# Optimization experiments

Hardware: AMD Instinct MI355X
Metric: run time of the kernel (lower is better)

Reference implementation:

```python
import jax, jax.numpy as jnp
import numpy as np

HIDDEN = 1024
HEADS = 16
HEAD_DIM = HIDDEN // HEADS


def setup_inputs() -> dict:
    key = jax.random.key(0)
    kx, kw = jax.random.split(key)
    x = jax.random.normal(kx, (1, 4096, HIDDEN), dtype=jnp.float32)
    # torch Linear weight is [out, in]; we store as [in, out] for x @ W
    W_qkv = jax.random.normal(kw, (HIDDEN, 3 * HIDDEN), dtype=jnp.float32) * (HIDDEN ** -0.5)
    return {"x": x, "W_qkv": W_qkv}


def reference(x, W_qkv):
    B, T, _ = x.shape
    qkv = x @ W_qkv                                    # [B, T, 3*HIDDEN]
    qkv = qkv.reshape(B, T, 3, HEADS, HEAD_DIM)
    qkv = jnp.transpose(qkv, (2, 0, 3, 1, 4))          # [3, B, H, T, Dh]
    q, k, v = qkv[0], qkv[1], qkv[2]
    scale = HEAD_DIM ** -0.5
    attn = jnp.einsum("bhqd,bhkd->bhqk", q, k) * scale  # [B, H, T, T] materialized (naive)
    attn = jax.nn.softmax(attn, axis=-1)
    out = jnp.einsum("bhqk,bhkd->bhqd", attn, v)        # [B, H, T, Dh]
    out = jnp.transpose(out, (0, 2, 1, 3)).reshape(B, T, HIDDEN)
    return out
```

## Files before the change

kernel.cpp:

```cpp
#include <hip/hip_runtime.h>

#define SEQ 4096
#define HID 1024
#define NH  16
#define DH  64
#define N3  3072

typedef __attribute__((ext_vector_type(4))) float floatx4;
typedef __attribute__((ext_vector_type(8))) short shortx8;
typedef __attribute__((ext_vector_type(4))) short shortx4;

__device__ __forceinline__ short f2bf(float f) {
    return (short)((__builtin_bit_cast(unsigned, f) + 0x8000u) >> 16);
}
__device__ __forceinline__ unsigned pk2bf(float a, float b) {
    unsigned ua = __builtin_bit_cast(unsigned, a) + 0x8000u;
    unsigned ub = __builtin_bit_cast(unsigned, b) + 0x8000u;
    return (ua >> 16) | (ub & 0xFFFF0000u);
}
__device__ __forceinline__ shortx4 pk4bf(float a, float b, float c, float d) {
    union { unsigned u[2]; shortx4 s; } x;
    x.u[0] = pk2bf(a, b);
    x.u[1] = pk2bf(c, d);
    return x.s;
}

__device__ __forceinline__ unsigned cvtpk(float lo, float hi) {
    unsigned r;
    asm("v_cvt_pk_bf16_f32 %0, %1, %2" : "=v"(r) : "v"(lo), "v"(hi));
    return r;
}

#if __has_builtin(__builtin_amdgcn_exp2f)
#define fexp2 __builtin_amdgcn_exp2f
#else
#define fexp2 exp2f
#endif

#define mfma32 __builtin_amdgcn_mfma_f32_16x16x32_bf16

__device__ __forceinline__ void gll16(const short* g, short* l) {
    __builtin_amdgcn_global_load_lds(
        (const __attribute__((address_space(1))) unsigned*)g,
        (__attribute__((address_space(3))) unsigned*)l, 16, 0, 0);
}

__global__ __launch_bounds__(256) void prep(
    const float* __restrict__ x, const float* __restrict__ W,
    short* __restrict__ Xb, short* __restrict__ Wt)
{
    __shared__ short Ws[128 * 40];
    const int t = threadIdx.x;
    if (blockIdx.x < 4096) {
        size_t i = (size_t)blockIdx.x * 256 + t;
        float4 v = *(const float4*)&x[i * 4];
        *(shortx4*)&Xb[i * 4] = pk4bf(v.x, v.y, v.z, v.w);
        return;
    }
    const int bx = (int)blockIdx.x - 4096;
    const int n0 = (bx % 24) * 128;
    const int k0 = (bx / 24) * 32;
    #pragma unroll
    for (int i = 0; i < 4; i++) {
        int idx = t + i * 256;
        int k = idx >> 5, c4 = idx & 31;
        float4 v = *(const float4*)&W[(size_t)(k0 + k) * N3 + n0 + c4 * 4];
        Ws[(c4 * 4 + 0) * 40 + k] = f2bf(v.x);
        Ws[(c4 * 4 + 1) * 40 + k] = f2bf(v.y);
        Ws[(c4 * 4 + 2) * 40 + k] = f2bf(v.z);
        Ws[(c4 * 4 + 3) * 40 + k] = f2bf(v.w);
    }
    __syncthreads();
    #pragma unroll
    for (int i = 0; i < 2; i++) {
        int idx = t + i * 256;
        int n = idx >> 2, seg = idx & 3;
        shortx8 g = *(const shortx8*)&Ws[n * 40 + seg * 8];
        *(shortx8*)&Wt[(size_t)(n0 + n) * HID + k0 + seg * 8] = g;
    }
}

#define LDC 136
__global__ __launch_bounds__(256) void qkv_gemm(
    const short* __restrict__ Xb, const short* __restrict__ Wt,
    short* __restrict__ Qb, short* __restrict__ Kb, short* __restrict__ Vt)
{
    __shared__ short SM[18432];
    short* As = SM;
    short* Bs = SM + 128 * 64;
    const int tid  = threadIdx.x;
    const int m0   = blockIdx.x * 128;
    const int n0   = blockIdx.y * 128;
    const int lane = tid & 63;
    const int wid  = tid >> 6;
    const int wm   = (wid >> 1) * 64;
    const int wn   = (wid & 1) * 64;
    const int l15  = lane & 15;
    const int quad = lane >> 4;

    floatx4 acc[4][4];
    #pragma unroll
    for (int i = 0; i < 4; i++)
        #pragma unroll
        for (int j = 0; j < 4; j++)
            acc[i][j] = (floatx4){0.f, 0.f, 0.f, 0.f};

    const int arow = tid >> 3, ac = tid & 7;
    const int swk  = (ac ^ (arow & 7)) << 3;
    const short* ag = Xb + (size_t)(m0 + arow) * HID + swk;
    const short* bg = Wt + (size_t)(n0 + arow) * HID + swk;
    short* al = As + (size_t)(tid & 192) * 8;
    short* bl = Bs + (size_t)(tid & 192) * 8;
    const int r7 = l15 & 7;

    for (int k0 = 0; k0 < HID; k0 += 64) {
        #pragma unroll
        for (int i = 0; i < 4; i++)
            gll16(ag + (size_t)i * 32 * HID + k0, al + i * 2048);
        #pragma unroll
        for (int i = 0; i < 4; i++)
            gll16(bg + (size_t)i * 32 * HID + k0, bl + i * 2048);
        __syncthreads();
        #pragma unroll
        for (int kh = 0; kh < 2; kh++) {
            shortx8 af[4], bf[4];
            #pragma unroll
            for (int t = 0; t < 4; t++) {
                int R = wm + t * 16 + l15;
                af[t] = *(const shortx8*)&As[(R << 6) + ((((kh << 2) + quad) ^ r7) << 3)];
                int Rb = wn + t * 16 + l15;
                bf[t] = *(const shortx8*)&Bs[(Rb << 6) + ((((kh << 2) + quad) ^ r7) << 3)];
            }
            #pragma unroll
            for (int tm = 0; tm < 4; tm++)
                #pragma unroll
                for (int tn = 0; tn < 4; tn++)
                    acc[tm][tn] = mfma32(af[tm], bf[tn], acc[tm][tn], 0, 0, 0);
        }
        __syncthreads();
    }

    short* Cs = SM;
    const float sc = (n0 < 1024) ? 0.18033688011112042f : 1.0f;
    #pragma unroll
    for (int tm = 0; tm < 4; tm++)
        #pragma unroll
        for (int tn = 0; tn < 4; tn++)
            #pragma unroll
            for (int r = 0; r < 4; r++)
                Cs[(wm + tm * 16 + quad * 4 + r) * LDC + wn + tn * 16 + l15] =
                    f2bf(acc[tm][tn][r] * sc);
    __syncthreads();
    const int h0 = (n0 & 1023) >> 6;
    if (n0 < 2048) {
        short* base = (n0 < 1024) ? Qb : Kb;
        #pragma unroll
        for (int j = 0; j < 8; j++) {
            int idx = tid + j * 256;
            int row = idx >> 4, col = (idx & 15) * 8;
            shortx8 v = *(const shortx8*)&Cs[row * LDC + col];
            *(shortx8*)&base[((size_t)(h0 + (col >> 6)) * SEQ + m0 + row) * DH + (col & 63)] = v;
        }
    } else {
        #pragma unroll
        for (int j = 0; j < 8; j++) {
            int idx = tid + j * 256;
            int col = idx >> 4;
            int t8  = (idx & 15) * 8;
            shortx8 v;
            #pragma unroll
            for (int k = 0; k < 8; k++) v[k] = Cs[(t8 + k) * LDC + col];
            *(shortx8*)&Vt[((size_t)(h0 + (col >> 6)) * DH + (col & 63)) * SEQ + m0 + t8] = v;
        }
    }
}

__global__ __launch_bounds__(256, 3) void flash_attn(
    const short* __restrict__ Qb, const short* __restrict__ Kb,
    const short* __restrict__ Vt, float* __restrict__ out,
    float* __restrict__ Opart, float* __restrict__ Lpart,
    int chn, int final)
{
    __shared__ short Ks[2][4096];
    __shared__ short Vs[2][4096];
    const int tid  = threadIdx.x;
    const int wid  = tid >> 6;
    const int lane = tid & 63;
    const int l15  = lane & 15;
    const int quad = lane >> 4;

    const int nblk = (int)(gridDim.x * gridDim.y * gridDim.z);
    const int lin  = (int)blockIdx.x + ((int)blockIdx.y << 4) + ((int)blockIdx.z << 8);
    const int work = (lin & 7) * (nblk >> 3) + (lin >> 3);
    const int h    = (work >> 4) & 15;
    const int ch   = work >> 8;
    const int q0   = (work & 15) * 256 + wid * 64;
    const int nit    = (chn == 1) ? 64 : (ch == 0 ? 22 : 21);
    const int tstart = (chn == 1) ? 0  : (ch == 0 ? 0 : 1408 + (ch - 1) * 1344);
    const shortx8 ones8 = {(short)0x3F80, (short)0x3F80, (short)0x3F80, (short)0x3F80,
                           (short)0x3F80, (short)0x3F80, (short)0x3F80, (short)0x3F80};
    const floatx4 z4 = {0.f, 0.f, 0.f, 0.f};

    shortx8 qf[4][2];
    #pragma unroll
    for (int s = 0; s < 4; s++) {
        const short* qp = Qb + ((size_t)h * SEQ + q0 + s * 16 + l15) * DH;
        qf[s][0] = *(const shortx8*)(qp + quad * 8);
        qf[s][1] = *(const shortx8*)(qp + 32 + quad * 8);
    }

    floatx4 oacc[4][4];
    #pragma unroll
    for (int s = 0; s < 4; s++)
        #pragma unroll
        for (int dn = 0; dn < 4; dn++)
            oacc[s][dn] = z4;
    floatx4 lacc[4] = {z4, z4, z4, z4};

    const int rK   = tid >> 3, sK = tid & 7;
    const int key0 = 8 * ((rK >> 2) & 3) + 4 * ((rK >> 4) & 1) + (rK & 3);
    const int swo  = (sK ^ (rK & 7)) << 3;
    const short* kg = Kb + ((size_t)h * SEQ + tstart + key0) * DH + swo;
    const short* vg = Vt + ((size_t)h * DH + rK) * SEQ + tstart + swo;
    const int wslot = (tid & 192) * 8;

#define STAGE(b) do { \
        gll16(kg,            &Ks[b][wslot]); \
        gll16(kg + 32 * DH,  &Ks[b][wslot + 2048]); \
        gll16(vg,            &Vs[b][wslot]); \
        gll16(vg + 32 * SEQ, &Vs[b][wslot + 2048]); \
    } while (0)

    STAGE(0);
    kg += 64 * DH;  vg += 64;

    for (int it = 0; it < nit; it++) {
        __syncthreads();
        if (it + 1 < nit) {
            int b = (it + 1) & 1;
            STAGE(b);
            kg += 64 * DH;  vg += 64;
        }
        const short* ks = Ks[it & 1];
        const short* vs = Vs[it & 1];

        #pragma unroll
        for (int pair = 0; pair < 2; pair++) {
            int Ra = (pair * 2) * 16 + l15;
            int Rb = Ra + 16;
            int offa = (Ra << 6) + ((quad ^ (Ra & 7)) << 3);
            int offb = (Rb << 6) + ((quad ^ (Rb & 7)) << 3);
            shortx8 kf0a = *(const shortx8*)&ks[offa];
            shortx8 kf1a = *(const shortx8*)&ks[offa ^ 32];
            shortx8 kf0b = *(const shortx8*)&ks[offb];
            shortx8 kf1b = *(const shortx8*)&ks[offb ^ 32];
            floatx4 sta[4], stb[4];
            __builtin_amdgcn_s_setprio(1);
            #pragma unroll
            for (int s = 0; s < 4; s++) {
                floatx4 a = mfma32(kf0a, qf[s][0], z4, 0, 0, 0);
                a = mfma32(kf1a, qf[s][1], a, 0, 0, 0);
                sta[s] = a;
                floatx4 b = mfma32(kf0b, qf[s][0], z4, 0, 0, 0);
                b = mfma32(kf1b, qf[s][1], b, 0, 0, 0);
                stb[s] = b;
            }
            __builtin_amdgcn_s_setprio(0);
            union { unsigned u[4]; shortx8 s8; } pa[4];
            #pragma unroll
            for (int s = 0; s < 4; s++) {
                pa[s].u[0] = cvtpk(fexp2(sta[s][0]), fexp2(sta[s][1]));
                pa[s].u[1] = cvtpk(fexp2(sta[s][2]), fexp2(sta[s][3]));
                pa[s].u[2] = cvtpk(fexp2(stb[s][0]), fexp2(stb[s][1]));
                pa[s].u[3] = cvtpk(fexp2(stb[s][2]), fexp2(stb[s][3]));
            }
            __builtin_amdgcn_s_setprio(1);
            #pragma unroll
            for (int s = 0; s < 4; s++)
                lacc[s] = mfma32(pa[s].s8, ones8, lacc[s], 0, 0, 0);
            #pragma unroll
            for (int dn = 0; dn < 4; dn++) {
                int row = dn * 16 + l15;
                int off = ((row << 6) + ((quad ^ (row & 7)) << 3)) ^ (pair << 5);
                shortx8 vv = *(const shortx8*)&vs[off];
                #pragma unroll
                for (int s = 0; s < 4; s++)
                    oacc[s][dn] = mfma32(pa[s].s8, vv, oacc[s][dn], 0, 0, 0);
            }
            __builtin_amdgcn_s_setprio(0);
        }
    }
#undef STAGE

    if (final) {
        #pragma unroll
        for (int s = 0; s < 4; s++)
            #pragma unroll
            for (int r = 0; r < 4; r++) {
                float rl = 1.0f / lacc[s][r];
                int query = q0 + s * 16 + quad * 4 + r;
                float* d = out + (size_t)query * HID + h * DH + l15;
                #pragma unroll
                for (int dn = 0; dn < 4; dn++)
                    d[dn * 16] = oacc[s][dn][r] * rl;
            }
    } else {
        #pragma unroll
        for (int s = 0; s < 4; s++)
            #pragma unroll
            for (int r = 0; r < 4; r++) {
                int query = q0 + s * 16 + quad * 4 + r;
                float* d = Opart + ((size_t)ch * SEQ + query) * HID + h * DH + l15;
                #pragma unroll
                for (int dn = 0; dn < 4; dn++)
                    d[dn * 16] = oacc[s][dn][r];
            }
        if (l15 == 0) {
            float* lp = Lpart + ((size_t)ch * NH + h) * SEQ + q0;
            #pragma unroll
            for (int s = 0; s < 4; s++)
                #pragma unroll
                for (int r = 0; r < 4; r++)
                    lp[s * 16 + quad * 4 + r] = lacc[s][r];
        }
    }
}

__global__ __launch_bounds__(256) void combine(
    const float* __restrict__ Opart, const float* __restrict__ Lpart,
    float* __restrict__ out, int chn)
{
    size_t i = ((size_t)blockIdx.x * 256 + threadIdx.x) * 4;
    int q = (int)(i >> 10);
    int h = ((int)i & 1023) >> 6;
    float4 o = {0.f, 0.f, 0.f, 0.f};
    float l = 0.f;
    for (int c = 0; c < chn; c++) {
        float4 p = *(const float4*)&Opart[(size_t)c * SEQ * HID + i];
        o.x += p.x; o.y += p.y; o.z += p.z; o.w += p.w;
        l += Lpart[((size_t)c * NH + h) * SEQ + q];
    }
    float rl = 1.0f / l;
    float4 r = {o.x * rl, o.y * rl, o.z * rl, o.w * rl};
    *(float4*)&out[i] = r;
}

extern "C" void kernel_launch(void* const* d_in, const int* in_sizes, int n_in,
                              void* d_out, int out_size, void* d_ws, size_t ws_size,
                              hipStream_t stream) {
    const float* x = (const float*)d_in[0];
    const float* W = (const float*)d_in[1];
    float* out = (float*)d_out;

    short* Xb = (short*)d_ws;
    short* Wt = Xb + (size_t)SEQ * HID;
    short* Qb = Wt + (size_t)N3 * HID;
    short* Kb = Qb + (size_t)NH * SEQ * DH;
    short* Vt = Kb + (size_t)NH * SEQ * DH;
    float* Opart = (float*)(Vt + (size_t)NH * SEQ * DH);

    const size_t need3 = 39845888ull
                       + 3ull * SEQ * HID * 4
                       + 3ull * NH * SEQ * 4;
    const int chn = (ws_size >= need3) ? 3 : 1;
    float* Lpart = Opart + (size_t)chn * SEQ * HID;

    prep      <<<dim3(4096 + 768), 256, 0, stream>>>(x, W, Xb, Wt);
    qkv_gemm  <<<dim3(SEQ / 128, N3 / 128), 256, 0, stream>>>(Xb, Wt, Qb, Kb, Vt);
    flash_attn<<<dim3(SEQ / 256, NH, chn), 256, 0, stream>>>(
        Qb, Kb, Vt, out, Opart, Lpart, chn, chn == 1);
    if (chn > 1)
        combine<<<dim3(SEQ * HID / 1024), 256, 0, stream>>>(Opart, Lpart, out, chn);
}
```

Baseline: 195.7 us.

## Fuse split-KV combine into flash_attn via atomic last-block reduction and swizzle GEMM grid

Removes the separate combine kernel. Each flash_attn block now bumps a per-(head, query-tile) atomic counter after writing its partial output, and the last of the chn chunks to arrive reduces the partials and writes the normalized output. A memset of the counters is added before the attention launch. The qkv_gemm block index is also remapped so that consecutive blocks spread across XCD-strided tiles, aiming at better L2 locality. The trade is one fewer kernel launch and one less full pass over the partials, at the cost of a memset, threadfences, and a serial tail inside the last-arriving block.

```diff
diff --git a/kernel.cpp b/kernel.cpp
--- a/kernel.cpp
+++ b/kernel.cpp
@@ -89,8 +89,10 @@
     short* As = SM;
     short* Bs = SM + 128 * 64;
     const int tid  = threadIdx.x;
-    const int m0   = blockIdx.x * 128;
-    const int n0   = blockIdx.y * 128;
+    const int lin  = (int)blockIdx.x + (int)blockIdx.y * 32;
+    const int w    = (lin & 7) * 96 + (lin >> 3);
+    const int m0   = (w & 31) * 128;
+    const int n0   = (w >> 5) * 128;
     const int lane = tid & 63;
     const int wid  = tid >> 6;
     const int wm   = (wid >> 1) * 64;
@@ -179,7 +181,7 @@
     const short* __restrict__ Qb, const short* __restrict__ Kb,
     const short* __restrict__ Vt, float* __restrict__ out,
     float* __restrict__ Opart, float* __restrict__ Lpart,
-    int chn, int final)
+    int* __restrict__ cnt, int chn, int final)
 {
     __shared__ short Ks[2][4096];
     __shared__ short Vs[2][4096];
@@ -304,45 +306,54 @@
                 for (int dn = 0; dn < 4; dn++)
                     d[dn * 16] = oacc[s][dn][r] * rl;
             }
-    } else {
+        return;
+    }
+
+    #pragma unroll
+    for (int s = 0; s < 4; s++)
+        #pragma unroll
+        for (int r = 0; r < 4; r++) {
+            int query = q0 + s * 16 + quad * 4 + r;
+            float* d = Opart + ((size_t)ch * SEQ + query) * HID + h * DH + l15;
+            #pragma unroll
+            for (int dn = 0; dn < 4; dn++)
+                d[dn * 16] = oacc[s][dn][r];
+        }
+    if (l15 == 0) {
+        float* lp = Lpart + ((size_t)ch * NH + h) * SEQ + q0;
         #pragma unroll
         for (int s = 0; s < 4; s++)
             #pragma unroll
-            for (int r = 0; r < 4; r++) {
-                int query = q0 + s * 16 + quad * 4 + r;
-                float* d = Opart + ((size_t)ch * SEQ + query) * HID + h * DH + l15;
-                #pragma unroll
-                for (int dn = 0; dn < 4; dn++)
-                    d[dn * 16] = oacc[s][dn][r];
-            }
-        if (l15 == 0) {
-            float* lp = Lpart + ((size_t)ch * NH + h) * SEQ + q0;
-            #pragma unroll
-            for (int s = 0; s < 4; s++)
-                #pragma unroll
-                for (int r = 0; r < 4; r++)
-                    lp[s * 16 + quad * 4 + r] = lacc[s][r];
-        }
-    }
-}
-
-__global__ __launch_bounds__(256) void combine(
-    const float* __restrict__ Opart, const float* __restrict__ Lpart,
-    float* __restrict__ out, int chn)
-{
-    size_t i = ((size_t)blockIdx.x * 256 + threadIdx.x) * 4;
-    int q = (int)(i >> 10);
-    int h = ((int)i & 1023) >> 6;
-    float4 o = {0.f, 0.f, 0.f, 0.f};
-    float l = 0.f;
-    for (int c = 0; c < chn; c++) {
-        float4 p = *(const float4*)&Opart[(size_t)c * SEQ * HID + i];
-        o.x += p.x; o.y += p.y; o.z += p.z; o.w += p.w;
-        l += Lpart[((size_t)c * NH + h) * SEQ + q];
-    }
-    float rl = 1.0f / l;
-    float4 r = {o.x * rl, o.y * rl, o.z * rl, o.w * rl};
-    *(float4*)&out[i] = r;
+            for (int r = 0; r < 4; r++)
+                lp[s * 16 + quad * 4 + r] = lacc[s][r];
+    }
+
+    __threadfence();
+    __shared__ int sdone;
+    __syncthreads();
+    if (tid == 0) sdone = atomicAdd(&cnt[work & 255], 1);
+    __syncthreads();
+    if (sdone == chn - 1) {
+        __threadfence();
+        const int qb0 = (work & 15) * 256;
+        #pragma unroll 4
+        for (int j = 0; j < 16; j++) {
+            int idx = j * 256 + tid;
+            int q   = qb0 + (idx >> 4);
+            int d4  = (idx & 15) * 4;
+            size_t off = (size_t)q * HID + h * DH + d4;
+            float4 o = {0.f, 0.f, 0.f, 0.f};
+            float lsum = 0.f;
+            for (int c = 0; c < chn; c++) {
+                float4 p = *(const float4*)&Opart[(size_t)c * SEQ * HID + off];
+                o.x += p.x; o.y += p.y; o.z += p.z; o.w += p.w;
+                lsum += Lpart[((size_t)c * NH + h) * SEQ + q];
+            }
+            float rl = 1.0f / lsum;
+            float4 r = {o.x * rl, o.y * rl, o.z * rl, o.w * rl};
+            *(float4*)&out[off] = r;
+        }
+    }
 }
 
 extern "C" void kernel_launch(void* const* d_in, const int* in_sizes, int n_in,
@@ -361,14 +372,16 @@
 
     const size_t need3 = 39845888ull
                        + 3ull * SEQ * HID * 4
-                       + 3ull * NH * SEQ * 4;
+                       + 3ull * NH * SEQ * 4
+                       + 1024;
     const int chn = (ws_size >= need3) ? 3 : 1;
     float* Lpart = Opart + (size_t)chn * SEQ * HID;
+    int*   cnt   = (int*)(Lpart + (size_t)chn * NH * SEQ);
 
     prep      <<<dim3(4096 + 768), 256, 0, stream>>>(x, W, Xb, Wt);
     qkv_gemm  <<<dim3(SEQ / 128, N3 / 128), 256, 0, stream>>>(Xb, Wt, Qb, Kb, Vt);
+    if (chn > 1)
+        hipMemsetAsync(cnt, 0, 256 * sizeof(int), stream);
     flash_attn<<<dim3(SEQ / 256, NH, chn), 256, 0, stream>>>(
-        Qb, Kb, Vt, out, Opart, Lpart, chn, chn == 1);
-    if (chn > 1)
-        combine<<<dim3(SEQ * HID / 1024), 256, 0, stream>>>(Opart, Lpart, out, chn);
-}
+        Qb, Kb, Vt, out, Opart, Lpart, cnt, chn, chn == 1);
+}
```

New measurement: 323.1 us. +65.1%, slower.
